# Performance work log

Hardware: AMD Instinct MI355X
Metric: run time of the kernel (lower is better)

## Reference

```python
import jax, jax.numpy as jnp
import numpy as np

NENV, SEQ, LATENT = 4096, 128, 64
EMB, HID = 256, 1024
SA = 2  # state_action_size


def setup_inputs() -> dict:
    key = jax.random.key(0)
    ks = jax.random.split(key, 8)
    def w(k, shape):
        return (jax.random.normal(k, shape, jnp.float32) / np.sqrt(shape[0])).astype(jnp.float32)
    return {
        "z": jax.random.normal(ks[0], (NENV, SEQ, LATENT), jnp.float32),
        "rnn_hxs": jnp.zeros((NENV, HID), jnp.float32),
        "w1": w(ks[1], (SA + LATENT, 32)), "b1": jnp.zeros((32,), jnp.float32),
        "w2": w(ks[2], (32, EMB)),          "b2": jnp.zeros((EMB,), jnp.float32),
        "wih": w(ks[3], (EMB, 3 * HID)),    "bih": jnp.zeros((3 * HID,), jnp.float32),
        "whh": w(ks[4], (HID, 3 * HID)),    "bhh": jnp.zeros((3 * HID,), jnp.float32),
        "w3": w(ks[5], (HID, HID // 2)),    "b3": jnp.zeros((HID // 2,), jnp.float32),
        "w4": w(ks[6], (HID // 2, SA)),     "b4": jnp.zeros((SA,), jnp.float32),
    }


def _gru_cell(x, h, wih, whh, bih, bhh):
    # PyTorch nn.GRU single-step semantics.
    gi = x @ wih + bih                    # [n, 3H]
    gh = h @ whh + bhh                    # [n, 3H]
    i_r, i_z, i_n = jnp.split(gi, 3, axis=-1)
    h_r, h_z, h_n = jnp.split(gh, 3, axis=-1)
    r = jax.nn.sigmoid(i_r + h_r)
    u = jax.nn.sigmoid(i_z + h_z)
    n = jnp.tanh(i_n + r * h_n)
    return (1.0 - u) * n + u * h


def reference(z, rnn_hxs, w1, b1, w2, b2, wih, bih, whh, bhh, w3, b3, w4, b4):
    zt = jnp.transpose(z, (1, 0, 2))                     # [S, N, latent]
    state0 = -2.0 * jnp.ones((z.shape[0], SA), z.dtype)  # initial fake action/state

    def step(carry, z_t):
        state, h = carry
        x = jnp.concatenate([state, z_t], axis=-1)       # [N, 2+latent]
        x = jax.nn.relu(x @ w1 + b1)
        x = jax.nn.relu(x @ w2 + b2)                     # mlp_in -> [N, EMB]
        h = _gru_cell(x, h, wih, whh, bih, bhh)          # [N, HID]
        o = jax.nn.relu(h @ w3 + b3)
        o = jnp.tanh(o @ w4 + b4)                        # output_linear -> [N, 2]
        return (o, h), o

    (_, h_new), outs = jax.lax.scan(step, (state0, rnn_hxs), zt)
    # original returns outputs.permute(1,0,2) -> [nenv, seq, 2], plus new hidden
    return jnp.transpose(outs, (1, 0, 2)), h_new
```

## Files before the change

kernel.cpp:

```cpp
#include <hip/hip_runtime.h>
#include <cstdint>
#include <cstddef>

#define NENV 4096
#define SEQ  128
#define LATENT 64
#define EMB  256
#define HID  1024
#define SA   2

typedef _Float16 half8 __attribute__((ext_vector_type(8)));
typedef float f32x4 __attribute__((ext_vector_type(4)));

__device__ __forceinline__ float sigmoid_f(float x){ return 1.0f/(1.0f + __expf(-x)); }

__device__ __forceinline__ void dma16(const void* g, void* l){
  __builtin_amdgcn_global_load_lds(
      (const __attribute__((address_space(1))) void*)g,
      (__attribute__((address_space(3))) void*)l, 16, 0, 0);
}

__device__ __forceinline__ f32x4 mfma16(half8 a, half8 b, f32x4 c){
  return __builtin_amdgcn_mfma_f32_16x16x32_f16(a, b, c, 0, 0, 0);
}

__global__ void transpose_cvt_kernel(const float* __restrict__ in, _Float16* __restrict__ out,
                                     int K, int C){
  int n = K*C;
  for (int i = blockIdx.x*blockDim.x + threadIdx.x; i < n; i += gridDim.x*blockDim.x){
    int c = i / K;
    int k = i - c*K;
    out[i] = (_Float16)in[(size_t)k*C + c];
  }
}

__global__ void init_h_kernel(const float* __restrict__ rnn, _Float16* __restrict__ h16){
  int n = NENV*HID;
  for (int i = blockIdx.x*blockDim.x + threadIdx.x; i < n; i += gridDim.x*blockDim.x){
    h16[i] = (_Float16)rnn[i];
  }
}

__device__ __forceinline__ void gru_phase(
    const _Float16* __restrict__ A, const _Float16* __restrict__ W, int K,
    int r0, int c0, int tid, int wave, int m, int q, int n0,
    half8* sA, half8* sB, f32x4* accR, f32x4* accZ, f32x4* accN)
{
  const int row64 = tid >> 2, seg = tid & 3;
  const _Float16* gA0 = A + (size_t)(r0 +  0 + row64)*K +  0 + seg*8;
  const _Float16* gA1 = A + (size_t)(r0 + 64 + row64)*K +  0 + seg*8;
  const _Float16* gA2 = A + (size_t)(r0 +  0 + row64)*K + 32 + seg*8;
  const _Float16* gA3 = A + (size_t)(r0 + 64 + row64)*K + 32 + seg*8;
  const _Float16* gB0 = W + (size_t)(0*HID + c0 + row64)*K +  0 + seg*8;
  const _Float16* gB1 = W + (size_t)(0*HID + c0 + row64)*K + 32 + seg*8;
  const _Float16* gB2 = W + (size_t)(1*HID + c0 + row64)*K +  0 + seg*8;
  const _Float16* gB3 = W + (size_t)(1*HID + c0 + row64)*K + 32 + seg*8;
  const _Float16* gB4 = W + (size_t)(2*HID + c0 + row64)*K +  0 + seg*8;
  const _Float16* gB5 = W + (size_t)(2*HID + c0 + row64)*K + 32 + seg*8;

  char* dA0 = (char*)&sA[0*256 + wave*64];
  char* dA1 = (char*)&sA[1*256 + wave*64];
  char* dA2 = (char*)&sA[2*256 + wave*64];
  char* dA3 = (char*)&sA[3*256 + wave*64];
  char* dB0 = (char*)&sB[0*256 + wave*64];
  char* dB1 = (char*)&sB[1*256 + wave*64];
  char* dB2 = (char*)&sB[2*256 + wave*64];
  char* dB3 = (char*)&sB[3*256 + wave*64];
  char* dB4 = (char*)&sB[4*256 + wave*64];
  char* dB5 = (char*)&sB[5*256 + wave*64];

  for (int k0 = 0; k0 < K; k0 += 64){
    dma16(gA0, dA0); dma16(gA1, dA1); dma16(gA2, dA2); dma16(gA3, dA3);
    dma16(gB0, dB0); dma16(gB1, dB1); dma16(gB2, dB2);
    dma16(gB3, dB3); dma16(gB4, dB4); dma16(gB5, dB5);
    gA0 += 64; gA1 += 64; gA2 += 64; gA3 += 64;
    gB0 += 64; gB1 += 64; gB2 += 64; gB3 += 64; gB4 += 64; gB5 += 64;
    __syncthreads();
#pragma unroll
    for (int c = 0; c < 2; ++c){
      half8 b0 = sB[0*512 + c*256 + (n0+m)*4 + q];
      half8 b1 = sB[1*512 + c*256 + (n0+m)*4 + q];
      half8 b2 = sB[2*512 + c*256 + (n0+m)*4 + q];
#pragma unroll
      for (int mt = 0; mt < 8; ++mt){
        half8 a = sA[c*512 + (mt*16 + m)*4 + q];
        accR[mt] = mfma16(a, b0, accR[mt]);
        accZ[mt] = mfma16(a, b1, accZ[mt]);
        accN[mt] = mfma16(a, b2, accN[mt]);
      }
    }
    __syncthreads();
  }
}

__global__ __launch_bounds__(256, 2) void gru_kernel(
    const _Float16* __restrict__ x2h, const _Float16* __restrict__ hcur,
    const _Float16* __restrict__ wihT, const _Float16* __restrict__ whhT,
    const float* __restrict__ bih, const float* __restrict__ bhh,
    _Float16* __restrict__ hnxt, float* __restrict__ hout)
{
  __shared__ half8 sA[1024];
  __shared__ half8 sB[1536];
  const int tid = threadIdx.x;
  const int lane = tid & 63, wave = tid >> 6;
  const int m = lane & 15, q = lane >> 4, n0 = wave*16;

  const int id = blockIdx.x;
  const int colg = (id & 7)*2 + ((id >> 3) & 1);
  const int rowg = id >> 4;
  const int r0 = rowg*128, c0 = colg*64;

  f32x4 accR[8], accZ[8], accNi[8], accNh[8];
#pragma unroll
  for (int i = 0; i < 8; ++i){
    accR[i] = (f32x4){0.f,0.f,0.f,0.f};
    accZ[i] = (f32x4){0.f,0.f,0.f,0.f};
    accNi[i] = (f32x4){0.f,0.f,0.f,0.f};
    accNh[i] = (f32x4){0.f,0.f,0.f,0.f};
  }

  gru_phase(x2h,  wihT, EMB, r0, c0, tid, wave, m, q, n0, sA, sB, accR, accZ, accNi);
  gru_phase(hcur, whhT, HID, r0, c0, tid, wave, m, q, n0, sA, sB, accR, accZ, accNh);

  const int gc = c0 + n0 + m;
  const float b_r  = bih[gc]         + bhh[gc];
  const float b_z  = bih[gc + HID]   + bhh[gc + HID];
  const float b_in = bih[gc + 2*HID];
  const float b_hn = bhh[gc + 2*HID];
#pragma unroll
  for (int mt = 0; mt < 8; ++mt){
#pragma unroll
    for (int r = 0; r < 4; ++r){
      int grow = r0 + mt*16 + q*4 + r;
      float rr = sigmoid_f(accR[mt][r] + b_r);
      float u  = sigmoid_f(accZ[mt][r] + b_z);
      float nn = tanhf(accNi[mt][r] + b_in + rr*(accNh[mt][r] + b_hn));
      size_t idx = (size_t)grow*HID + gc;
      float hold = (float)hcur[idx];
      float hnew = (1.0f - u)*nn + u*hold;
      hnxt[idx] = (_Float16)hnew;
      if (hout) hout[idx] = hnew;
    }
  }
}

__global__ __launch_bounds__(256, 2) void out1_kernel(
    const _Float16* __restrict__ h16, const _Float16* __restrict__ w3T,
    const float* __restrict__ b3, _Float16* __restrict__ o1)
{
  __shared__ half8 sA[1024];
  __shared__ half8 sB[512];
  const int tid = threadIdx.x;
  const int lane = tid & 63, wave = tid >> 6;
  const int m = lane & 15, q = lane >> 4, n0 = wave*16;
  const int row64 = tid >> 2, seg = tid & 3;

  const int id = blockIdx.x;
  const int colg = id & 7;
  const int rowg = id >> 3;
  const int r0 = rowg*128, c0 = colg*64;

  f32x4 acc[8];
#pragma unroll
  for (int i = 0; i < 8; ++i) acc[i] = (f32x4){0.f,0.f,0.f,0.f};

  const _Float16* gA0 = h16 + (size_t)(r0 +  0 + row64)*HID +  0 + seg*8;
  const _Float16* gA1 = h16 + (size_t)(r0 + 64 + row64)*HID +  0 + seg*8;
  const _Float16* gA2 = h16 + (size_t)(r0 +  0 + row64)*HID + 32 + seg*8;
  const _Float16* gA3 = h16 + (size_t)(r0 + 64 + row64)*HID + 32 + seg*8;
  const _Float16* gB0 = w3T + (size_t)(c0 + row64)*HID +  0 + seg*8;
  const _Float16* gB1 = w3T + (size_t)(c0 + row64)*HID + 32 + seg*8;

  char* dA0 = (char*)&sA[0*256 + wave*64];
  char* dA1 = (char*)&sA[1*256 + wave*64];
  char* dA2 = (char*)&sA[2*256 + wave*64];
  char* dA3 = (char*)&sA[3*256 + wave*64];
  char* dB0 = (char*)&sB[0*256 + wave*64];
  char* dB1 = (char*)&sB[1*256 + wave*64];

  for (int k0 = 0; k0 < HID; k0 += 64){
    dma16(gA0, dA0); dma16(gA1, dA1); dma16(gA2, dA2); dma16(gA3, dA3);
    dma16(gB0, dB0); dma16(gB1, dB1);
    gA0 += 64; gA1 += 64; gA2 += 64; gA3 += 64; gB0 += 64; gB1 += 64;
    __syncthreads();
#pragma unroll
    for (int c = 0; c < 2; ++c){
      half8 b = sB[c*256 + (n0+m)*4 + q];
#pragma unroll
      for (int mt = 0; mt < 8; ++mt){
        half8 a = sA[c*512 + (mt*16 + m)*4 + q];
        acc[mt] = mfma16(a, b, acc[mt]);
      }
    }
    __syncthreads();
  }

  const int gc = c0 + n0 + m;
  const float bb = b3[gc];
#pragma unroll
  for (int mt = 0; mt < 8; ++mt){
#pragma unroll
    for (int r = 0; r < 4; ++r){
      int grow = r0 + mt*16 + q*4 + r;
      o1[(size_t)grow*(HID/2) + gc] = (_Float16)fmaxf(acc[mt][r] + bb, 0.f);
    }
  }
}

__global__ void tail_head_kernel(
    const _Float16* __restrict__ o1, const float* __restrict__ w4, const float* __restrict__ b4,
    const float* __restrict__ z,  const float* __restrict__ w1, const float* __restrict__ b1,
    const float* __restrict__ w2, const float* __restrict__ b2,
    _Float16* __restrict__ x2h, float* __restrict__ out, int t, int mode)
{
  __shared__ float sw2[32*256];
  __shared__ float sw1[66*32];
  __shared__ float sz[16][64];
  __shared__ float sx1[16][32];
  __shared__ float sst[16][2];
  const int tid = threadIdx.x;
  const int r0 = blockIdx.x*16;

  if (mode != 2){
    for (int i = tid; i < 66*32; i += 256) sw1[i] = w1[i];
    for (int i = tid; i < 32*256; i += 256) sw2[i] = w2[i];
    int zt = (mode == 0) ? 0 : (t + 1);
    for (int i = tid; i < 16*64; i += 256){
      int r = i >> 6, k = i & 63;
      sz[r][k] = z[(size_t)(r0 + r)*SEQ*LATENT + zt*LATENT + k];
    }
  }

  if (mode != 0){
    int r = tid >> 4, p = tid & 15;
    const _Float16* orow = o1 + (size_t)(r0 + r)*(HID/2);
    float a0 = 0.f, a1 = 0.f;
    for (int k = p*32; k < p*32 + 32; ++k){
      float v = (float)orow[k];
      a0 += v*w4[k*2];
      a1 += v*w4[k*2 + 1];
    }
#pragma unroll
    for (int off = 1; off < 16; off <<= 1){
      a0 += __shfl_xor(a0, off);
      a1 += __shfl_xor(a1, off);
    }
    if (p == 0){
      a0 = tanhf(a0 + b4[0]);
      a1 = tanhf(a1 + b4[1]);
      out[(size_t)(r0 + r)*SEQ*SA + t*SA + 0] = a0;
      out[(size_t)(r0 + r)*SEQ*SA + t*SA + 1] = a1;
      sst[r][0] = a0; sst[r][1] = a1;
    }
  } else {
    if (tid < 32) sst[tid >> 1][tid & 1] = -2.0f;
  }
  __syncthreads();

  if (mode != 2){
    for (int it = tid; it < 16*32; it += 256){
      int r = it >> 5, j = it & 31;
      float acc = b1[j];
      acc += sst[r][0]*sw1[0*32 + j] + sst[r][1]*sw1[1*32 + j];
#pragma unroll 8
      for (int k = 0; k < 64; ++k) acc += sz[r][k]*sw1[(k + 2)*32 + j];
      sx1[r][j] = fmaxf(acc, 0.f);
    }
    __syncthreads();
    int col = tid;
    for (int r = 0; r < 16; ++r){
      float acc = b2[col];
#pragma unroll
      for (int k = 0; k < 32; ++k) acc += sx1[r][k]*sw2[k*256 + col];
      x2h[(size_t)(r0 + r)*EMB + col] = (_Float16)fmaxf(acc, 0.f);
    }
  }
}

extern "C" void kernel_launch(void* const* d_in, const int* in_sizes, int n_in,
                              void* d_out, int out_size, void* d_ws, size_t ws_size,
                              hipStream_t stream) {
  const float* z   = (const float*)d_in[0];
  const float* rnn = (const float*)d_in[1];
  const float* w1  = (const float*)d_in[2];
  const float* b1  = (const float*)d_in[3];
  const float* w2  = (const float*)d_in[4];
  const float* b2  = (const float*)d_in[5];
  const float* wih = (const float*)d_in[6];
  const float* bih = (const float*)d_in[7];
  const float* whh = (const float*)d_in[8];
  const float* bhh = (const float*)d_in[9];
  const float* w3  = (const float*)d_in[10];
  const float* b3  = (const float*)d_in[11];
  const float* w4  = (const float*)d_in[12];
  const float* b4  = (const float*)d_in[13];
  float* out = (float*)d_out;

  char* ws = (char*)d_ws;
  _Float16* wihT = (_Float16*)ws;                 ws += (size_t)3*HID*EMB*2;
  _Float16* whhT = (_Float16*)ws;                 ws += (size_t)3*HID*HID*2;
  _Float16* w3T  = (_Float16*)ws;                 ws += (size_t)(HID/2)*HID*2;
  _Float16* h16a = (_Float16*)ws;                 ws += (size_t)NENV*HID*2;
  _Float16* h16b = (_Float16*)ws;                 ws += (size_t)NENV*HID*2;
  _Float16* x2h  = (_Float16*)ws;                 ws += (size_t)NENV*EMB*2;
  _Float16* o1   = (_Float16*)ws;                 ws += (size_t)NENV*(HID/2)*2;

  transpose_cvt_kernel<<<512, 256, 0, stream>>>(wih, wihT, EMB, 3*HID);
  transpose_cvt_kernel<<<1024, 256, 0, stream>>>(whh, whhT, HID, 3*HID);
  transpose_cvt_kernel<<<256, 256, 0, stream>>>(w3, w3T, HID, HID/2);
  init_h_kernel<<<1024, 256, 0, stream>>>(rnn, h16a);

  tail_head_kernel<<<NENV/16, 256, 0, stream>>>(o1, w4, b4, z, w1, b1, w2, b2, x2h, out, 0, 0);

  float* hfinal = out + (size_t)NENV*SEQ*SA;
  for (int t = 0; t < SEQ; ++t){
    _Float16* hc = (t & 1) ? h16b : h16a;
    _Float16* hn = (t & 1) ? h16a : h16b;
    gru_kernel<<<512, 256, 0, stream>>>(x2h, hc, wihT, whhT, bih, bhh, hn,
                                        (t == SEQ - 1) ? hfinal : nullptr);
    out1_kernel<<<256, 256, 0, stream>>>(hn, w3T, b3, o1);
    tail_head_kernel<<<NENV/16, 256, 0, stream>>>(o1, w4, b4, z, w1, b1, w2, b2, x2h, out,
                                                  t, (t < SEQ - 1) ? 1 : 2);
  }
}
```

Before: 10.91 ms.

## Fuse per-step GRU, output and head kernels into one persistent kernel

Replaces the 384 per-timestep kernel launches with a single persistent kernel of 512 blocks that loops over the sequence and synchronises with a spin-wait atomic grid barrier. The output GEMM is retiled to 64-row tiles so all 512 blocks have work, and the head MLP keeps its weights in LDS for the whole kernel, with w2 stored as fp16. This removes launch gaps and repeated weight loads at the cost of three grid barriers per step. It relies on all 512 blocks being co-resident (2 per CU). The barrier has a timeout guard that could silently break correctness if that assumption fails.

```diff
diff --git a/kernel.cpp b/kernel.cpp
--- a/kernel.cpp
+++ b/kernel.cpp
@@ -8,6 +8,7 @@
 #define EMB  256
 #define HID  1024
 #define SA   2
+#define GRID 512
 
 typedef _Float16 half8 __attribute__((ext_vector_type(8)));
 typedef float f32x4 __attribute__((ext_vector_type(4)));
@@ -22,6 +23,34 @@
 
 __device__ __forceinline__ f32x4 mfma16(half8 a, half8 b, f32x4 c){
   return __builtin_amdgcn_mfma_f32_16x16x32_f16(a, b, c, 0, 0, 0);
+}
+
+struct SMemG { half8 sA[1024]; half8 sB[1536]; };
+struct SMemO { half8 sA[512];  half8 sB[512];  };
+struct SMem {
+  float     sw1[66*32];
+  _Float16  sw2h[32*256];
+  float     sb1[32];
+  float     sb2[256];
+  union { SMemG g; SMemO o; } u;
+  float sst[8][2];
+  float sx1[8][32];
+};
+static_assert(sizeof(SMem) <= 80*1024, "LDS over budget for 2 blocks/CU");
+
+__device__ __forceinline__ void gbar(int* cnt, int& ep){
+  __syncthreads();
+  if (threadIdx.x == 0){
+    ep += GRID;
+    __hip_atomic_fetch_add(cnt, 1, __ATOMIC_RELEASE, __HIP_MEMORY_SCOPE_AGENT);
+    long guard = 0;
+    while (__hip_atomic_load(cnt, __ATOMIC_RELAXED, __HIP_MEMORY_SCOPE_AGENT) < ep){
+      __builtin_amdgcn_s_sleep(2);
+      if (++guard > (1L<<27)) break;
+    }
+  }
+  __syncthreads();
+  __builtin_amdgcn_fence(__ATOMIC_ACQUIRE, "agent");
 }
 
 __global__ void transpose_cvt_kernel(const float* __restrict__ in, _Float16* __restrict__ out,
@@ -41,7 +70,7 @@
   }
 }
 
-__device__ __forceinline__ void gru_phase(
+__device__ __forceinline__ void gru_kphase(
     const _Float16* __restrict__ A, const _Float16* __restrict__ W, int K,
     int r0, int c0, int tid, int wave, int m, int q, int n0,
     half8* sA, half8* sB, f32x4* accR, f32x4* accZ, f32x4* accN)
@@ -93,18 +122,15 @@
   }
 }
 
-__global__ __launch_bounds__(256, 2) void gru_kernel(
+__device__ void gru_block(
     const _Float16* __restrict__ x2h, const _Float16* __restrict__ hcur,
     const _Float16* __restrict__ wihT, const _Float16* __restrict__ whhT,
     const float* __restrict__ bih, const float* __restrict__ bhh,
-    _Float16* __restrict__ hnxt, float* __restrict__ hout)
-{
-  __shared__ half8 sA[1024];
-  __shared__ half8 sB[1536];
+    _Float16* __restrict__ hnxt, float* __restrict__ hout, SMem& s)
+{
   const int tid = threadIdx.x;
   const int lane = tid & 63, wave = tid >> 6;
   const int m = lane & 15, q = lane >> 4, n0 = wave*16;
-
   const int id = blockIdx.x;
   const int colg = (id & 7)*2 + ((id >> 3) & 1);
   const int rowg = id >> 4;
@@ -119,8 +145,8 @@
     accNh[i] = (f32x4){0.f,0.f,0.f,0.f};
   }
 
-  gru_phase(x2h,  wihT, EMB, r0, c0, tid, wave, m, q, n0, sA, sB, accR, accZ, accNi);
-  gru_phase(hcur, whhT, HID, r0, c0, tid, wave, m, q, n0, sA, sB, accR, accZ, accNh);
+  gru_kphase(x2h,  wihT, EMB, r0, c0, tid, wave, m, q, n0, s.u.g.sA, s.u.g.sB, accR, accZ, accNi);
+  gru_kphase(hcur, whhT, HID, r0, c0, tid, wave, m, q, n0, s.u.g.sA, s.u.g.sB, accR, accZ, accNh);
 
   const int gc = c0 + n0 + m;
   const float b_r  = bih[gc]         + bhh[gc];
@@ -144,51 +170,45 @@
   }
 }
 
-__global__ __launch_bounds__(256, 2) void out1_kernel(
+__device__ void out1_block(
     const _Float16* __restrict__ h16, const _Float16* __restrict__ w3T,
-    const float* __restrict__ b3, _Float16* __restrict__ o1)
-{
-  __shared__ half8 sA[1024];
-  __shared__ half8 sB[512];
+    const float* __restrict__ b3, _Float16* __restrict__ o1, SMem& s)
+{
+  half8* sA = s.u.o.sA;
+  half8* sB = s.u.o.sB;
   const int tid = threadIdx.x;
   const int lane = tid & 63, wave = tid >> 6;
   const int m = lane & 15, q = lane >> 4, n0 = wave*16;
-  const int row64 = tid >> 2, seg = tid & 3;
-
+  const int row = tid >> 2, seg = tid & 3;
   const int id = blockIdx.x;
   const int colg = id & 7;
   const int rowg = id >> 3;
-  const int r0 = rowg*128, c0 = colg*64;
-
-  f32x4 acc[8];
-#pragma unroll
-  for (int i = 0; i < 8; ++i) acc[i] = (f32x4){0.f,0.f,0.f,0.f};
-
-  const _Float16* gA0 = h16 + (size_t)(r0 +  0 + row64)*HID +  0 + seg*8;
-  const _Float16* gA1 = h16 + (size_t)(r0 + 64 + row64)*HID +  0 + seg*8;
-  const _Float16* gA2 = h16 + (size_t)(r0 +  0 + row64)*HID + 32 + seg*8;
-  const _Float16* gA3 = h16 + (size_t)(r0 + 64 + row64)*HID + 32 + seg*8;
-  const _Float16* gB0 = w3T + (size_t)(c0 + row64)*HID +  0 + seg*8;
-  const _Float16* gB1 = w3T + (size_t)(c0 + row64)*HID + 32 + seg*8;
+  const int r0 = rowg*64, c0 = colg*64;
+
+  f32x4 acc[4];
+#pragma unroll
+  for (int i = 0; i < 4; ++i) acc[i] = (f32x4){0.f,0.f,0.f,0.f};
+
+  const _Float16* gA0 = h16 + (size_t)(r0 + row)*HID +  0 + seg*8;
+  const _Float16* gA1 = h16 + (size_t)(r0 + row)*HID + 32 + seg*8;
+  const _Float16* gB0 = w3T + (size_t)(c0 + row)*HID +  0 + seg*8;
+  const _Float16* gB1 = w3T + (size_t)(c0 + row)*HID + 32 + seg*8;
 
   char* dA0 = (char*)&sA[0*256 + wave*64];
   char* dA1 = (char*)&sA[1*256 + wave*64];
-  char* dA2 = (char*)&sA[2*256 + wave*64];
-  char* dA3 = (char*)&sA[3*256 + wave*64];
   char* dB0 = (char*)&sB[0*256 + wave*64];
   char* dB1 = (char*)&sB[1*256 + wave*64];
 
   for (int k0 = 0; k0 < HID; k0 += 64){
-    dma16(gA0, dA0); dma16(gA1, dA1); dma16(gA2, dA2); dma16(gA3, dA3);
-    dma16(gB0, dB0); dma16(gB1, dB1);
-    gA0 += 64; gA1 += 64; gA2 += 64; gA3 += 64; gB0 += 64; gB1 += 64;
+    dma16(gA0, dA0); dma16(gA1, dA1); dma16(gB0, dB0); dma16(gB1, dB1);
+    gA0 += 64; gA1 += 64; gB0 += 64; gB1 += 64;
     __syncthreads();
 #pragma unroll
     for (int c = 0; c < 2; ++c){
       half8 b = sB[c*256 + (n0+m)*4 + q];
 #pragma unroll
-      for (int mt = 0; mt < 8; ++mt){
-        half8 a = sA[c*512 + (mt*16 + m)*4 + q];
+      for (int mt = 0; mt < 4; ++mt){
+        half8 a = sA[c*256 + (mt*16 + m)*4 + q];
         acc[mt] = mfma16(a, b, acc[mt]);
       }
     }
@@ -198,7 +218,7 @@
   const int gc = c0 + n0 + m;
   const float bb = b3[gc];
 #pragma unroll
-  for (int mt = 0; mt < 8; ++mt){
+  for (int mt = 0; mt < 4; ++mt){
 #pragma unroll
     for (int r = 0; r < 4; ++r){
       int grow = r0 + mt*16 + q*4 + r;
@@ -207,73 +227,104 @@
   }
 }
 
-__global__ void tail_head_kernel(
-    const _Float16* __restrict__ o1, const float* __restrict__ w4, const float* __restrict__ b4,
-    const float* __restrict__ z,  const float* __restrict__ w1, const float* __restrict__ b1,
-    const float* __restrict__ w2, const float* __restrict__ b2,
-    _Float16* __restrict__ x2h, float* __restrict__ out, int t, int mode)
-{
-  __shared__ float sw2[32*256];
-  __shared__ float sw1[66*32];
-  __shared__ float sz[16][64];
-  __shared__ float sx1[16][32];
-  __shared__ float sst[16][2];
+__device__ void tail_head_block(
+    const _Float16* __restrict__ o1, const float* __restrict__ z,
+    const float* __restrict__ w4, const float* __restrict__ b4,
+    float* __restrict__ out, _Float16* __restrict__ x2h,
+    int t, bool do_out, bool do_head, SMem& s)
+{
   const int tid = threadIdx.x;
-  const int r0 = blockIdx.x*16;
-
-  if (mode != 2){
-    for (int i = tid; i < 66*32; i += 256) sw1[i] = w1[i];
-    for (int i = tid; i < 32*256; i += 256) sw2[i] = w2[i];
-    int zt = (mode == 0) ? 0 : (t + 1);
-    for (int i = tid; i < 16*64; i += 256){
-      int r = i >> 6, k = i & 63;
-      sz[r][k] = z[(size_t)(r0 + r)*SEQ*LATENT + zt*LATENT + k];
-    }
-  }
-
-  if (mode != 0){
-    int r = tid >> 4, p = tid & 15;
-    const _Float16* orow = o1 + (size_t)(r0 + r)*(HID/2);
+  const int r0c = blockIdx.x*8;
+  if (do_out){
+    int row = tid >> 5, p = tid & 31;
+    const _Float16* orow = o1 + (size_t)(r0c + row)*(HID/2);
+    half8 v0 = *(const half8*)(orow + p*16);
+    half8 v1 = *(const half8*)(orow + p*16 + 8);
+    const float2* w4v = (const float2*)w4;
     float a0 = 0.f, a1 = 0.f;
-    for (int k = p*32; k < p*32 + 32; ++k){
-      float v = (float)orow[k];
-      a0 += v*w4[k*2];
-      a1 += v*w4[k*2 + 1];
-    }
-#pragma unroll
-    for (int off = 1; off < 16; off <<= 1){
-      a0 += __shfl_xor(a0, off);
-      a1 += __shfl_xor(a1, off);
+#pragma unroll
+    for (int i = 0; i < 8; ++i){
+      float f = (float)v0[i]; float2 w = w4v[p*16 + i];
+      a0 += f*w.x; a1 += f*w.y;
+    }
+#pragma unroll
+    for (int i = 0; i < 8; ++i){
+      float f = (float)v1[i]; float2 w = w4v[p*16 + 8 + i];
+      a0 += f*w.x; a1 += f*w.y;
+    }
+#pragma unroll
+    for (int off = 1; off < 32; off <<= 1){
+      a0 += __shfl_xor(a0, off, 32);
+      a1 += __shfl_xor(a1, off, 32);
     }
     if (p == 0){
       a0 = tanhf(a0 + b4[0]);
       a1 = tanhf(a1 + b4[1]);
-      out[(size_t)(r0 + r)*SEQ*SA + t*SA + 0] = a0;
-      out[(size_t)(r0 + r)*SEQ*SA + t*SA + 1] = a1;
-      sst[r][0] = a0; sst[r][1] = a1;
+      out[(size_t)(r0c + row)*SEQ*SA + t*SA + 0] = a0;
+      out[(size_t)(r0c + row)*SEQ*SA + t*SA + 1] = a1;
+      s.sst[row][0] = a0; s.sst[row][1] = a1;
     }
   } else {
-    if (tid < 32) sst[tid >> 1][tid & 1] = -2.0f;
+    if (tid < 16) s.sst[tid >> 1][tid & 1] = -2.0f;
   }
   __syncthreads();
 
-  if (mode != 2){
-    for (int it = tid; it < 16*32; it += 256){
-      int r = it >> 5, j = it & 31;
-      float acc = b1[j];
-      acc += sst[r][0]*sw1[0*32 + j] + sst[r][1]*sw1[1*32 + j];
+  if (do_head){
+    const int zt = do_out ? (t + 1) : 0;
+    int row = tid >> 5, col = tid & 31;
+    const float* zr = z + (size_t)(r0c + row)*SEQ*LATENT + zt*LATENT;
+    float acc = s.sb1[col] + s.sst[row][0]*s.sw1[col] + s.sst[row][1]*s.sw1[32 + col];
 #pragma unroll 8
-      for (int k = 0; k < 64; ++k) acc += sz[r][k]*sw1[(k + 2)*32 + j];
-      sx1[r][j] = fmaxf(acc, 0.f);
-    }
-    __syncthreads();
-    int col = tid;
-    for (int r = 0; r < 16; ++r){
-      float acc = b2[col];
-#pragma unroll
-      for (int k = 0; k < 32; ++k) acc += sx1[r][k]*sw2[k*256 + col];
-      x2h[(size_t)(r0 + r)*EMB + col] = (_Float16)fmaxf(acc, 0.f);
-    }
+    for (int k = 0; k < 64; ++k) acc += zr[k]*s.sw1[(k + 2)*32 + col];
+    s.sx1[row][col] = fmaxf(acc, 0.f);
+    __syncthreads();
+    int c = tid;
+#pragma unroll
+    for (int r = 0; r < 8; ++r){
+      float acc2 = s.sb2[c];
+#pragma unroll
+      for (int k = 0; k < 32; ++k) acc2 += s.sx1[r][k]*(float)s.sw2h[k*256 + c];
+      x2h[(size_t)(r0c + r)*EMB + c] = (_Float16)fmaxf(acc2, 0.f);
+    }
+    __syncthreads();
+  }
+}
+
+__global__ __launch_bounds__(256, 2) void persist_kernel(
+    const float* __restrict__ z,
+    const _Float16* __restrict__ wihT, const _Float16* __restrict__ whhT,
+    const _Float16* __restrict__ w3T,
+    const float* __restrict__ bih, const float* __restrict__ bhh,
+    const float* __restrict__ b3,
+    const float* __restrict__ w1, const float* __restrict__ b1,
+    const float* __restrict__ w2, const float* __restrict__ b2,
+    const float* __restrict__ w4, const float* __restrict__ b4,
+    _Float16* __restrict__ h16a, _Float16* __restrict__ h16b,
+    _Float16* __restrict__ x2h, _Float16* __restrict__ o1,
+    float* __restrict__ out, float* __restrict__ hfinal,
+    int* __restrict__ bar)
+{
+  __shared__ SMem s;
+  const int tid = threadIdx.x;
+  for (int i = tid; i < 66*32; i += 256) s.sw1[i] = w1[i];
+  for (int i = tid; i < 32*256; i += 256) s.sw2h[i] = (_Float16)w2[i];
+  if (tid < 32) s.sb1[tid] = b1[tid];
+  s.sb2[tid] = b2[tid];
+  __syncthreads();
+
+  int ep = 0;
+  tail_head_block(o1, z, w4, b4, out, x2h, 0, false, true, s);
+  gbar(bar, ep);
+
+  for (int t = 0; t < SEQ; ++t){
+    const _Float16* hc = (t & 1) ? h16b : h16a;
+    _Float16* hn = (t & 1) ? h16a : h16b;
+    gru_block(x2h, hc, wihT, whhT, bih, bhh, hn, (t == SEQ-1) ? hfinal : nullptr, s);
+    gbar(bar, ep);
+    out1_block(hn, w3T, b3, o1, s);
+    gbar(bar, ep);
+    tail_head_block(o1, z, w4, b4, out, x2h, t, true, t < SEQ-1, s);
+    if (t < SEQ-1) gbar(bar, ep);
   }
 }
 
@@ -304,22 +355,16 @@
   _Float16* h16b = (_Float16*)ws;                 ws += (size_t)NENV*HID*2;
   _Float16* x2h  = (_Float16*)ws;                 ws += (size_t)NENV*EMB*2;
   _Float16* o1   = (_Float16*)ws;                 ws += (size_t)NENV*(HID/2)*2;
-
+  int*      bar  = (int*)ws;                      ws += 256;
+
+  hipMemsetAsync(bar, 0, 256, stream);
   transpose_cvt_kernel<<<512, 256, 0, stream>>>(wih, wihT, EMB, 3*HID);
   transpose_cvt_kernel<<<1024, 256, 0, stream>>>(whh, whhT, HID, 3*HID);
   transpose_cvt_kernel<<<256, 256, 0, stream>>>(w3, w3T, HID, HID/2);
   init_h_kernel<<<1024, 256, 0, stream>>>(rnn, h16a);
 
-  tail_head_kernel<<<NENV/16, 256, 0, stream>>>(o1, w4, b4, z, w1, b1, w2, b2, x2h, out, 0, 0);
-
   float* hfinal = out + (size_t)NENV*SEQ*SA;
-  for (int t = 0; t < SEQ; ++t){
-    _Float16* hc = (t & 1) ? h16b : h16a;
-    _Float16* hn = (t & 1) ? h16a : h16b;
-    gru_kernel<<<512, 256, 0, stream>>>(x2h, hc, wihT, whhT, bih, bhh, hn,
-                                        (t == SEQ - 1) ? hfinal : nullptr);
-    out1_kernel<<<256, 256, 0, stream>>>(hn, w3T, b3, o1);
-    tail_head_kernel<<<NENV/16, 256, 0, stream>>>(o1, w4, b4, z, w1, b1, w2, b2, x2h, out,
-                                                  t, (t < SEQ - 1) ? 1 : 2);
-  }
-}
+  persist_kernel<<<GRID, 256, 0, stream>>>(
+      z, wihT, whhT, w3T, bih, bhh, b3, w1, b1, w2, b2, w4, b4,
+      h16a, h16b, x2h, o1, out, hfinal, bar);
+}
```

Result: slower. 28.83 ms (+164.3%).
